# Optimization experiments

Hardware: AMD Instinct MI355X
Metric: run time of the kernel (lower is better)

Reference implementation:

```python
import jax, jax.numpy as jnp
import numpy as np

B = 2
D_MODEL = 256
D_FFN = 1024
N_LEVELS = 4
N_HEADS = 8
N_POINTS = 4
D_HEAD = D_MODEL // N_HEADS
SHAPES = np.array([[128, 128], [64, 64], [32, 32], [16, 16]], dtype=np.int32)  # (H, W) per level
LEN = int(SHAPES.prod(axis=1).sum())  # 21760
EPS = 1e-5


def _layer_norm(x, g, b):
    m = jnp.mean(x, axis=-1, keepdims=True)
    v = jnp.mean(jnp.square(x - m), axis=-1, keepdims=True)
    return (x - m) * jax.lax.rsqrt(v + EPS) * g + b


def _bilinear_gather(v_l, loc, H, W):
    # v_l: [B, H*W, NH, DH]; loc: [B, L, NH, NP, 2] in normalized [0,1] coords (x, y)
    # grid_sample(align_corners=False, padding_mode=zeros) semantics: pixel = loc * size - 0.5
    x = loc[..., 0] * W - 0.5
    y = loc[..., 1] * H - 0.5
    x0 = jnp.floor(x)
    y0 = jnp.floor(y)
    dx = x - x0
    dy = y - y0
    x0i = x0.astype(jnp.int32)
    y0i = y0.astype(jnp.int32)
    b_ix = jnp.arange(v_l.shape[0])[:, None, None, None]
    h_ix = jnp.arange(v_l.shape[2])[None, None, :, None]

    def corner(xi, yi, w):
        valid = (xi >= 0) & (xi < W) & (yi >= 0) & (yi < H)
        idx = jnp.clip(yi, 0, H - 1) * W + jnp.clip(xi, 0, W - 1)
        v = v_l[b_ix, idx, h_ix]  # [B, L, NH, NP, DH]
        return v * (w * valid.astype(v.dtype))[..., None]

    return (corner(x0i, y0i, (1 - dx) * (1 - dy))
            + corner(x0i + 1, y0i, dx * (1 - dy))
            + corner(x0i, y0i + 1, (1 - dx) * dy)
            + corner(x0i + 1, y0i + 1, dx * dy))


def _forward(src, pos, reference_points,
             w_off, b_off, w_attn, b_attn, w_val, b_val, w_out, b_out,
             ln1_g, ln1_b, w1, b1, w2, b2, ln2_g, ln2_b,
             spatial_shapes, level_start_index, padding_mask):
    shapes = np.asarray(spatial_shapes)        # static per-level (H, W)
    starts = np.asarray(level_start_index)     # static level offsets
    Bsz, L, _ = src.shape

    # ---- MSDeformAttn ----
    q = src + pos                              # with_pos_embed
    value = src @ w_val + b_val
    value = jnp.where(padding_mask[..., None], 0.0, value)
    value = value.reshape(Bsz, L, N_HEADS, D_HEAD)

    off = (q @ w_off + b_off).reshape(Bsz, L, N_HEADS, N_LEVELS, N_POINTS, 2)
    attn = (q @ w_attn + b_attn).reshape(Bsz, L, N_HEADS, N_LEVELS * N_POINTS)
    attn = jax.nn.softmax(attn, axis=-1).reshape(Bsz, L, N_HEADS, N_LEVELS, N_POINTS)

    wh = jnp.asarray(shapes[:, ::-1].copy(), dtype=src.dtype)  # [NL, 2] = (W, H)
    loc = reference_points[:, :, None, :, None, :] + off / wh[None, None, None, :, None, :]

    out = jnp.zeros((Bsz, L, N_HEADS, D_HEAD), src.dtype)
    for l in range(N_LEVELS):
        H, W = int(shapes[l, 0]), int(shapes[l, 1])
        s = int(starts[l])
        v_l = value[:, s:s + H * W]                          # [B, H*W, NH, DH]
        sampled = _bilinear_gather(v_l, loc[:, :, :, l], H, W)  # [B, L, NH, NP, DH]
        out = out + (sampled * attn[:, :, :, l][..., None]).sum(axis=3)
    attn_out = out.reshape(Bsz, L, D_MODEL) @ w_out + b_out

    # ---- residual + LN + FFN + residual + LN (dropout = identity in eval) ----
    x = _layer_norm(src + attn_out, ln1_g, ln1_b)
    ffn = jax.nn.relu(x @ w1 + b1) @ w2 + b2
    return _layer_norm(x + ffn, ln2_g, ln2_b)


def setup_inputs() -> dict:
    key = jax.random.key(0)
    ks = jax.random.split(key, 16)
    s = 0.02
    n_off = N_HEADS * N_LEVELS * N_POINTS
    level_start = np.concatenate([[0], SHAPES.prod(axis=1).cumsum()[:-1]]).astype(np.int32)
    return {
        "src": jax.random.normal(ks[0], (B, LEN, D_MODEL), jnp.float32),
        "pos": jax.random.normal(ks[1], (B, LEN, D_MODEL), jnp.float32),
        "reference_points": jax.random.uniform(ks[2], (B, LEN, N_LEVELS, 2), jnp.float32),
        "spatial_shapes": jnp.asarray(SHAPES),
        "level_start_index": jnp.asarray(level_start),
        "padding_mask": jnp.zeros((B, LEN), jnp.bool_),
        "w_off": jax.random.normal(ks[3], (D_MODEL, n_off * 2), jnp.float32) * s,
        "b_off": jax.random.normal(ks[4], (n_off * 2,), jnp.float32) * 0.5,
        "w_attn": jax.random.normal(ks[5], (D_MODEL, n_off), jnp.float32) * s,
        "b_attn": jnp.zeros((n_off,), jnp.float32),
        "w_val": jax.random.normal(ks[6], (D_MODEL, D_MODEL), jnp.float32) * s,
        "b_val": jnp.zeros((D_MODEL,), jnp.float32),
        "w_out": jax.random.normal(ks[7], (D_MODEL, D_MODEL), jnp.float32) * s,
        "b_out": jnp.zeros((D_MODEL,), jnp.float32),
        "ln1_g": jnp.ones((D_MODEL,), jnp.float32),
        "ln1_b": jnp.zeros((D_MODEL,), jnp.float32),
        "w1": jax.random.normal(ks[8], (D_MODEL, D_FFN), jnp.float32) * s,
        "b1": jnp.zeros((D_FFN,), jnp.float32),
        "w2": jax.random.normal(ks[9], (D_FFN, D_MODEL), jnp.float32) * s,
        "b2": jnp.zeros((D_MODEL,), jnp.float32),
        "ln2_g": jnp.ones((D_MODEL,), jnp.float32),
        "ln2_b": jnp.zeros((D_MODEL,), jnp.float32),
    }


def reference(src, pos, reference_points, spatial_shapes, level_start_index, padding_mask,
              w_off, b_off, w_attn, b_attn, w_val, b_val, w_out, b_out,
              ln1_g, ln1_b, w1, b1, w2, b2, ln2_g, ln2_b):
    return _forward(src, pos, reference_points,
                    w_off, b_off, w_attn, b_attn, w_val, b_val, w_out, b_out,
                    ln1_g, ln1_b, w1, b1, w2, b2, ln2_g, ln2_b,
                    spatial_shapes, level_start_index, padding_mask)
```

## Files before the change

kernel.cpp:

```cpp
#include <hip/hip_runtime.h>
#include <hip/hip_bf16.h>

#define BSZ      2
#define LTOK     21760
#define NTOK     (BSZ * LTOK)
#define DMODEL   256
#define DFFN     1024

typedef __attribute__((ext_vector_type(8))) short short8;
typedef __attribute__((ext_vector_type(4))) float f32x4;

__device__ __forceinline__ unsigned short f2bf(float x) {
    __hip_bfloat16 h = __float2bfloat16(x);
    return *reinterpret_cast<unsigned short*>(&h);
}
__device__ __forceinline__ float bf2f(unsigned short u) {
    union { unsigned int i; float f; } c; c.i = ((unsigned int)u) << 16; return c.f;
}
__device__ __forceinline__ float bflo(unsigned int u) {
    union { unsigned int i; float f; } c; c.i = u << 16; return c.f;
}
__device__ __forceinline__ float bfhi(unsigned int u) {
    union { unsigned int i; float f; } c; c.i = u & 0xffff0000u; return c.f;
}

#define TM 128
#define TN 256
#define TBK 32
#define EBS 264

__device__ __forceinline__ void gemm_core(
    const unsigned short* __restrict__ A,
    const unsigned short* __restrict__ Bt,
    unsigned short* sA, unsigned short* sB,
    int bm, int bn, int N, int K,
    int tid, int lane, int wm, int wn,
    f32x4 acc[4][8])
{
    const int sr = tid >> 6;
    const int fr = lane & 15;
    const int fk = (lane >> 4) * 8;

    for (int k0 = 0; k0 < K; k0 += TBK) {
        #pragma unroll
        for (int rr = 0; rr < 2; ++rr) {
            const int s = sr + rr * 4;
            const size_t grow = (size_t)(bm + s * 16 + fr);
            *(uint4*)&sA[s * 512 + lane * 8] = *(const uint4*)(A + grow * K + k0 + fk);
        }
        #pragma unroll
        for (int rr = 0; rr < 4; ++rr) {
            const int s = sr + rr * 4;
            int gn = bn + s * 16 + fr;
            gn = min(gn, N - 1);
            *(uint4*)&sB[s * 512 + lane * 8] = *(const uint4*)(Bt + (size_t)gn * K + k0 + fk);
        }
        __syncthreads();

        short8 af[4], bfr[8];
        #pragma unroll
        for (int i = 0; i < 4; ++i)
            af[i] = *(const short8*)&sA[(wm * 4 + i) * 512 + lane * 8];
        #pragma unroll
        for (int j = 0; j < 8; ++j)
            bfr[j] = *(const short8*)&sB[(wn * 8 + j) * 512 + lane * 8];
        #pragma unroll
        for (int i = 0; i < 4; ++i)
            #pragma unroll
            for (int j = 0; j < 8; ++j)
                acc[i][j] = __builtin_amdgcn_mfma_f32_16x16x32_bf16(
                    af[i], bfr[j], acc[i][j], 0, 0, 0);
        __syncthreads();
    }
}

__global__ __launch_bounds__(256, 2) void gemm_mfma(
    const unsigned short* __restrict__ A,
    const unsigned short* __restrict__ Bt, const float* __restrict__ bias,
    unsigned short* __restrict__ Cb,
    int M, int N, int K, int relu)
{
    __shared__ __align__(16) unsigned short smem[TM * TBK + TN * TBK];
    const int tid  = threadIdx.x;
    const int lane = tid & 63;
    const int wave = tid >> 6;
    const int wm = wave >> 1, wn = wave & 1;
    const int bm = blockIdx.y * TM;
    const int bn = blockIdx.x * TN;

    f32x4 acc[4][8];
    #pragma unroll
    for (int i = 0; i < 4; ++i)
        #pragma unroll
        for (int j = 0; j < 8; ++j)
            acc[i][j] = (f32x4){0.f, 0.f, 0.f, 0.f};

    gemm_core(A, Bt, smem, smem + TM * TBK, bm, bn, N, K, tid, lane, wm, wn, acc);

    const int r0 = (lane >> 4) * 4;
    const int c0 = lane & 15;
    unsigned short* eb = smem;
    #pragma unroll
    for (int i = 0; i < 4; ++i) {
        if (i) __syncthreads();
        #pragma unroll
        for (int j = 0; j < 8; ++j) {
            const int col = bn + wn * 128 + j * 16 + c0;
            const float bj = (col < N) ? bias[col] : 0.f;
            #pragma unroll
            for (int r = 0; r < 4; ++r) {
                float v = acc[i][j][r] + bj;
                if (relu) v = fmaxf(v, 0.f);
                eb[(wm * 16 + r0 + r) * EBS + wn * 128 + j * 16 + c0] = f2bf(v);
            }
        }
        __syncthreads();
        #pragma unroll
        for (int qq = 0; qq < 4; ++qq) {
            const int q  = tid + qq * 256;
            const int rl = q >> 5;
            const int ch = q & 31;
            const int grow = bm + (rl >> 4) * 64 + i * 16 + (rl & 15);
            const int colb = bn + ch * 8;
            if (colb < N)
                *(uint4*)&Cb[(size_t)grow * N + colb] =
                    *(const uint4*)&eb[rl * EBS + ch * 8];
        }
    }
}

__global__ __launch_bounds__(256, 2) void gemm_proj(
    const unsigned short* __restrict__ A0, const unsigned short* __restrict__ B0,
    const float* __restrict__ bias0, unsigned short* __restrict__ C0,
    const unsigned char* __restrict__ mask,
    const unsigned short* __restrict__ A1, const unsigned short* __restrict__ B1,
    const float* __restrict__ bias1, unsigned short* __restrict__ C1)
{
    __shared__ __align__(16) unsigned short smem[TM * TBK + TN * TBK];
    const int tid  = threadIdx.x;
    const int lane = tid & 63;
    const int wave = tid >> 6;
    const int wm = wave >> 1, wn = wave & 1;
    const int bm = blockIdx.y * TM;
    const int bx = blockIdx.x;

    const int isv = (bx == 0);
    const unsigned short* A    = isv ? A0 : A1;
    const unsigned short* Bt   = isv ? B0 : B1;
    const float*          bias = isv ? bias0 : bias1;
    const int N  = isv ? 256 : 384;
    const int bn = isv ? 0 : (bx - 1) * 256;
    const int K  = 256;

    f32x4 acc[4][8];
    #pragma unroll
    for (int i = 0; i < 4; ++i)
        #pragma unroll
        for (int j = 0; j < 8; ++j)
            acc[i][j] = (f32x4){0.f, 0.f, 0.f, 0.f};

    gemm_core(A, Bt, smem, smem + TM * TBK, bm, bn, N, K, tid, lane, wm, wn, acc);

    const int r0 = (lane >> 4) * 4;
    const int c0 = lane & 15;
    unsigned short* eb = smem;
    #pragma unroll
    for (int i = 0; i < 4; ++i) {
        if (i) __syncthreads();
        #pragma unroll
        for (int j = 0; j < 8; ++j) {
            const int col = bn + wn * 128 + j * 16 + c0;
            const float bj = (col < N) ? bias[col] : 0.f;
            #pragma unroll
            for (int r = 0; r < 4; ++r) {
                const int row = bm + wm * 64 + i * 16 + r0 + r;
                float v = acc[i][j][r] + bj;
                if (isv && mask[row]) v = 0.f;
                eb[(wm * 16 + r0 + r) * EBS + wn * 128 + j * 16 + c0] = f2bf(v);
            }
        }
        __syncthreads();
        #pragma unroll
        for (int qq = 0; qq < 4; ++qq) {
            const int q  = tid + qq * 256;
            const int rl = q >> 5;
            const int ch = q & 31;
            const int grow = bm + (rl >> 4) * 64 + i * 16 + (rl & 15);
            const int colb = bn + ch * 8;
            if (colb < N) {
                const uint4 val = *(const uint4*)&eb[rl * EBS + ch * 8];
                if (isv) {
                    const int bb   = grow >= LTOK;
                    const int srow = grow - bb * LTOK;
                    const int hcol = ch >> 2;
                    const int d    = (ch & 3) * 8;
                    *(uint4*)&C0[((size_t)(bb * 8 + hcol) * LTOK + srow) * 32 + d] = val;
                } else {
                    *(uint4*)&C1[(size_t)grow * 384 + colb] = val;
                }
            }
        }
    }
}

__global__ __launch_bounds__(256, 2) void gemm_ln(
    const unsigned short* __restrict__ A,
    const unsigned short* __restrict__ Bt, const float* __restrict__ bias,
    const unsigned short* __restrict__ resid,
    const float* __restrict__ g, const float* __restrict__ be,
    float* __restrict__ outF, unsigned short* __restrict__ outB, int K)
{
    __shared__ __align__(16) unsigned short smem[TM * TBK + TN * TBK];
    const int tid  = threadIdx.x;
    const int lane = tid & 63;
    const int wave = tid >> 6;
    const int wm = wave >> 1, wn = wave & 1;
    const int bm = blockIdx.y * TM;

    f32x4 acc[4][8];
    #pragma unroll
    for (int i = 0; i < 4; ++i)
        #pragma unroll
        for (int j = 0; j < 8; ++j)
            acc[i][j] = (f32x4){0.f, 0.f, 0.f, 0.f};

    gemm_core(A, Bt, smem, smem + TM * TBK, bm, 0, 256, K, tid, lane, wm, wn, acc);

    const int r0 = (lane >> 4) * 4;
    const int c0 = lane & 15;
    unsigned short* eb = smem;

    #pragma unroll
    for (int i = 0; i < 4; ++i) {
        if (i) __syncthreads();
        #pragma unroll
        for (int j = 0; j < 8; ++j) {
            const int col = wn * 128 + j * 16 + c0;
            const float bj = bias[col];
            #pragma unroll
            for (int r = 0; r < 4; ++r)
                eb[(wm * 16 + r0 + r) * EBS + col] = f2bf(acc[i][j][r] + bj);
        }
        __syncthreads();

        const int row = tid >> 3;
        const int l   = tid & 7;
        const int grow = bm + (row >> 4) * 64 + i * 16 + (row & 15);
        const unsigned short* rr = resid + (size_t)grow * 256 + l * 32;

        float s = 0.f, sq = 0.f;
        #pragma unroll
        for (int k = 0; k < 4; ++k) {
            const uint4 e = *(const uint4*)&eb[row * EBS + l * 32 + k * 8];
            const uint4 rv = *(const uint4*)(rr + k * 8);
            const unsigned int eu[4] = {e.x, e.y, e.z, e.w};
            const unsigned int ru[4] = {rv.x, rv.y, rv.z, rv.w};
            #pragma unroll
            for (int q = 0; q < 4; ++q) {
                const float v0 = bflo(eu[q]) + bflo(ru[q]);
                const float v1 = bfhi(eu[q]) + bfhi(ru[q]);
                s += v0 + v1;
                sq += v0 * v0 + v1 * v1;
            }
        }
        #pragma unroll
        for (int m = 4; m; m >>= 1) {
            s  += __shfl_xor(s, m, 8);
            sq += __shfl_xor(sq, m, 8);
        }
        const float mean = s * (1.f / 256.f);
        const float var  = sq * (1.f / 256.f) - mean * mean;
        const float rs   = rsqrtf(var + 1e-5f);

        #pragma unroll
        for (int k = 0; k < 4; ++k) {
            const int col = l * 32 + k * 8;
            const uint4 e = *(const uint4*)&eb[row * EBS + col];
            const uint4 rv = *(const uint4*)(rr + k * 8);
            const unsigned int eu[4] = {e.x, e.y, e.z, e.w};
            const unsigned int ru[4] = {rv.x, rv.y, rv.z, rv.w};
            float o[8];
            #pragma unroll
            for (int q = 0; q < 4; ++q) {
                const float g0 = g[col + q * 2],     b0 = be[col + q * 2];
                const float g1 = g[col + q * 2 + 1], b1 = be[col + q * 2 + 1];
                o[q * 2]     = (bflo(eu[q]) + bflo(ru[q]) - mean) * rs * g0 + b0;
                o[q * 2 + 1] = (bfhi(eu[q]) + bfhi(ru[q]) - mean) * rs * g1 + b1;
            }
            if (outB) {
                uint4 pk;
                pk.x = (unsigned)f2bf(o[0]) | ((unsigned)f2bf(o[1]) << 16);
                pk.y = (unsigned)f2bf(o[2]) | ((unsigned)f2bf(o[3]) << 16);
                pk.z = (unsigned)f2bf(o[4]) | ((unsigned)f2bf(o[5]) << 16);
                pk.w = (unsigned)f2bf(o[6]) | ((unsigned)f2bf(o[7]) << 16);
                *(uint4*)(outB + (size_t)grow * 256 + col) = pk;
            } else {
                float4 f0 = make_float4(o[0], o[1], o[2], o[3]);
                float4 f1 = make_float4(o[4], o[5], o[6], o[7]);
                *(float4*)(outF + (size_t)grow * 256 + col) = f0;
                *(float4*)(outF + (size_t)grow * 256 + col + 4) = f1;
            }
        }
        __syncthreads();
    }
}

__global__ __launch_bounds__(256) void prepass(
    const float* __restrict__ src, const float* __restrict__ pos,
    unsigned short* __restrict__ sb, unsigned short* __restrict__ qs)
{
    const size_t i = ((size_t)blockIdx.x * 256 + threadIdx.x) * 4;
    const float4 s = *(const float4*)(src + i);
    const float4 p = *(const float4*)(pos + i);
    ushort4 us, uq;
    us.x = f2bf(s.x); us.y = f2bf(s.y); us.z = f2bf(s.z); us.w = f2bf(s.w);
    uq.x = f2bf(s.x + p.x); uq.y = f2bf(s.y + p.y);
    uq.z = f2bf(s.z + p.z); uq.w = f2bf(s.w + p.w);
    *(ushort4*)(sb + i) = us;
    *(ushort4*)(qs + i) = uq;
}

__global__ void transpose_all(
    const float* __restrict__ w_val, const float* __restrict__ w_off,
    const float* __restrict__ w_att, const float* __restrict__ w_out,
    const float* __restrict__ w1,    const float* __restrict__ w2,
    const float* __restrict__ b_off, const float* __restrict__ b_att,
    unsigned short* __restrict__ wvalT, unsigned short* __restrict__ woaT,
    unsigned short* __restrict__ woutT, unsigned short* __restrict__ w1T,
    unsigned short* __restrict__ w2T,   float* __restrict__ bcat)
{
    const int blk = blockIdx.x;
    const int tx = threadIdx.x, ty = threadIdx.y;
    if (blk == 736) {
        const int t = ty * 32 + tx;
        bcat[t] = (t < 256) ? b_off[t] : b_att[t - 256];
        if (t + 256 < 384) bcat[t + 256] = b_att[t];
        return;
    }
    const float* W; unsigned short* Wt; int K, N, base;
    if      (blk < 64)  { W = w_val; Wt = wvalT;           K = 256;  N = 256;  base = 0;   }
    else if (blk < 128) { W = w_off; Wt = woaT;            K = 256;  N = 256;  base = 64;  }
    else if (blk < 160) { W = w_att; Wt = woaT + 256*256;  K = 256;  N = 128;  base = 128; }
    else if (blk < 224) { W = w_out; Wt = woutT;           K = 256;  N = 256;  base = 160; }
    else if (blk < 480) { W = w1;    Wt = w1T;             K = 256;  N = 1024; base = 224; }
    else                { W = w2;    Wt = w2T;             K = 1024; N = 256;  base = 480; }
    const int local = blk - base;
    const int kb = local % (K / 32);
    const int nb = local / (K / 32);
    const int k0 = kb * 32, n0 = nb * 32;

    __shared__ float t[32][33];
    #pragma unroll
    for (int i = 0; i < 32; i += 8)
        t[ty + i][tx] = W[(size_t)(k0 + ty + i) * N + n0 + tx];
    __syncthreads();
    #pragma unroll
    for (int i = 0; i < 32; i += 8)
        Wt[(size_t)(n0 + ty + i) * K + k0 + tx] = f2bf(t[tx][ty + i]);
}

__global__ __launch_bounds__(256) void sample_kernel(
    const unsigned short* __restrict__ vT, const unsigned short* __restrict__ qp,
    const float* __restrict__ ref,
    const int* __restrict__ sshapes, const int* __restrict__ lstart,
    unsigned short* __restrict__ samp)
{
    __shared__ __align__(16) int   s_o[256][4];
    __shared__ __align__(16) float s_w[256][4];

    const int blk   = blockIdx.x;
    const int plane = blk & 15;
    const int chunk = blk >> 4;
    const int b = plane >> 3;
    const int h = plane & 7;
    const int s0 = chunk * 16;
    const int t = threadIdx.x;

    {
        const int tl = t >> 4;
        const int p  = t & 15;
        const int l  = p >> 2;
        const int pp = p & 3;
        const int H = sshapes[2 * l], W = sshapes[2 * l + 1];
        const float Wf = (float)W, Hf = (float)H;
        const size_t tok = (size_t)(b * LTOK + s0 + tl);

        const float ox = bf2f(qp[tok * 384 + h * 32 + l * 8 + pp * 2 + 0]);
        const float oy = bf2f(qp[tok * 384 + h * 32 + l * 8 + pp * 2 + 1]);
        const float rx = ref[tok * 8 + l * 2 + 0];
        const float ry = ref[tok * 8 + l * 2 + 1];

        const float x = (rx + ox / Wf) * Wf - 0.5f;
        const float y = (ry + oy / Hf) * Hf - 0.5f;
        const float x0 = floorf(x), y0 = floorf(y);
        const float dx = x - x0, dy = y - y0;
        const int x0i = (int)x0, y0i = (int)y0;
        const int s = lstart[l];

        const float a = bf2f(qp[tok * 384 + 256 + h * 16 + p]);
        float mx = a;
        #pragma unroll
        for (int m = 8; m; m >>= 1) mx = fmaxf(mx, __shfl_xor(mx, m, 16));
        const float e = __expf(a - mx);
        float ssum = e;
        #pragma unroll
        for (int m = 8; m; m >>= 1) ssum += __shfl_xor(ssum, m, 16);
        const float prob = e / ssum;

        const float cw[4] = {(1.f - dx) * (1.f - dy), dx * (1.f - dy),
                             (1.f - dx) * dy,         dx * dy};
        const int cx[4] = {x0i, x0i + 1, x0i,     x0i + 1};
        const int cy[4] = {y0i, y0i,     y0i + 1, y0i + 1};
        int4   o4;
        float4 w4;
        #pragma unroll
        for (int c = 0; c < 4; ++c) {
            const bool valid = (cx[c] >= 0) & (cx[c] < W) & (cy[c] >= 0) & (cy[c] < H);
            const int xi = min(max(cx[c], 0), W - 1);
            const int yi = min(max(cy[c], 0), H - 1);
            ((int*)&o4)[c]   = (s + yi * W + xi) * 64;
            ((float*)&w4)[c] = valid ? cw[c] * prob : 0.f;
        }
        const int r = p * 16 + tl;
        *(int4*)&s_o[r][0]   = o4;
        *(float4*)&s_w[r][0] = w4;
    }
    __syncthreads();

    const int tl = t >> 4;
    const int dp = t & 15;
    const char* vp = (const char*)(vT + (size_t)plane * LTOK * 32) + dp * 4;
    float acc0 = 0.f, acc1 = 0.f;
    #pragma unroll
    for (int p = 0; p < 16; ++p) {
        const int r = p * 16 + tl;
        const int4   o4 = *(const int4*)&s_o[r][0];
        const float4 w4 = *(const float4*)&s_w[r][0];
        const unsigned int u0 = *(const unsigned int*)(vp + o4.x);
        const unsigned int u1 = *(const unsigned int*)(vp + o4.y);
        const unsigned int u2 = *(const unsigned int*)(vp + o4.z);
        const unsigned int u3 = *(const unsigned int*)(vp + o4.w);
        acc0 = fmaf(w4.x, bflo(u0), acc0); acc1 = fmaf(w4.x, bfhi(u0), acc1);
        acc0 = fmaf(w4.y, bflo(u1), acc0); acc1 = fmaf(w4.y, bfhi(u1), acc1);
        acc0 = fmaf(w4.z, bflo(u2), acc0); acc1 = fmaf(w4.z, bfhi(u2), acc1);
        acc0 = fmaf(w4.w, bflo(u3), acc0); acc1 = fmaf(w4.w, bfhi(u3), acc1);
    }
    const unsigned int o = (unsigned)f2bf(acc0) | ((unsigned)f2bf(acc1) << 16);
    *(unsigned int*)(samp + (size_t)(b * LTOK + s0 + tl) * 256 + h * 32 + dp * 2) = o;
}

extern "C" void kernel_launch(void* const* d_in, const int* in_sizes, int n_in,
                              void* d_out, int out_size, void* d_ws, size_t ws_size,
                              hipStream_t stream)
{
    const float* src   = (const float*)d_in[0];
    const float* pos   = (const float*)d_in[1];
    const float* ref   = (const float*)d_in[2];
    const int*   sshap = (const int*)d_in[3];
    const int*   lstrt = (const int*)d_in[4];
    const unsigned char* mask = (const unsigned char*)d_in[5];
    const float* w_off = (const float*)d_in[6];
    const float* b_off = (const float*)d_in[7];
    const float* w_att = (const float*)d_in[8];
    const float* b_att = (const float*)d_in[9];
    const float* w_val = (const float*)d_in[10];
    const float* b_val = (const float*)d_in[11];
    const float* w_out = (const float*)d_in[12];
    const float* b_out = (const float*)d_in[13];
    const float* ln1g  = (const float*)d_in[14];
    const float* ln1b  = (const float*)d_in[15];
    const float* w1    = (const float*)d_in[16];
    const float* b1    = (const float*)d_in[17];
    const float* w2    = (const float*)d_in[18];
    const float* b2    = (const float*)d_in[19];
    const float* ln2g  = (const float*)d_in[20];
    const float* ln2b  = (const float*)d_in[21];
    float* out = (float*)d_out;

    const size_t HSZ = (size_t)NTOK * 256 * 2;
    char* w = (char*)d_ws;
    unsigned short* qs     = (unsigned short*)w;
    unsigned short* samp16 = (unsigned short*)w;
    unsigned short* qpb    = (unsigned short*)(w + HSZ);
    unsigned short* vT     = (unsigned short*)(w + HSZ * 5 / 2);
    unsigned short* hidb   = (unsigned short*)w;
    unsigned short* sb     = (unsigned short*)(w + HSZ * 9 / 2);
    unsigned short* xb     = (unsigned short*)(w + HSZ * 11 / 2);
    char* wreg = w + HSZ * 13 / 2;
    unsigned short* wvalT  = (unsigned short*)wreg;
    unsigned short* woaT   = wvalT + 256 * 256;
    unsigned short* woutT  = woaT + 384 * 256;
    unsigned short* w1T    = woutT + 256 * 256;
    unsigned short* w2T    = w1T + 1024 * 256;
    float*          bcat   = (float*)(w2T + 256 * 1024);

    const dim3 blk(256);

    prepass<<<dim3(NTOK / 4), blk, 0, stream>>>(src, pos, sb, qs);

    transpose_all<<<dim3(737), dim3(32, 8), 0, stream>>>(
        w_val, w_off, w_att, w_out, w1, w2, b_off, b_att,
        wvalT, woaT, woutT, w1T, w2T, bcat);

    gemm_proj<<<dim3(3, NTOK / TM), blk, 0, stream>>>(
        sb, wvalT, b_val, vT, mask, qs, woaT, bcat, qpb);

    sample_kernel<<<dim3(16 * (LTOK / 16)), blk, 0, stream>>>(
        vT, qpb, ref, sshap, lstrt, samp16);

    gemm_ln<<<dim3(1, NTOK / TM), blk, 0, stream>>>(
        samp16, woutT, b_out, sb, ln1g, ln1b, nullptr, xb, 256);

    gemm_mfma<<<dim3(4, NTOK / TM), blk, 0, stream>>>(
        xb, w1T, b1, hidb, NTOK, DFFN, 256, 1);

    gemm_ln<<<dim3(1, NTOK / TM), blk, 0, stream>>>(
        hidb, w2T, b2, xb, ln2g, ln2b, out, nullptr, DFFN);
}
```

Baseline: 480.4 us.

## Replace LDS-staged GEMM tiles with direct-from-global per-wave MFMA tiles

All four GEMM kernels drop the shared-memory A/B staging loop with its block-wide barriers. Each wave now loads its 16-row A fragment and the B fragments straight from global memory (B through L2/cache) and runs MFMAs with smaller 64-row blocks. LDS is kept only as a per-wave epilogue buffer, which allows more blocks per CU and removes the __syncthreads. The cost is that B tiles are no longer shared across waves via LDS, so global/L2 traffic for weights rises, and reuse of each weight fragment goes down.

```diff
diff --git a/kernel.cpp b/kernel.cpp
--- a/kernel.cpp
+++ b/kernel.cpp
@@ -24,284 +24,243 @@
     union { unsigned int i; float f; } c; c.i = u & 0xffff0000u; return c.f;
 }
 
-#define TM 128
-#define TN 256
-#define TBK 32
-#define EBS 264
-
-__device__ __forceinline__ void gemm_core(
-    const unsigned short* __restrict__ A,
-    const unsigned short* __restrict__ Bt,
-    unsigned short* sA, unsigned short* sB,
-    int bm, int bn, int N, int K,
-    int tid, int lane, int wm, int wn,
-    f32x4 acc[4][8])
-{
-    const int sr = tid >> 6;
-    const int fr = lane & 15;
-    const int fk = (lane >> 4) * 8;
-
-    for (int k0 = 0; k0 < K; k0 += TBK) {
-        #pragma unroll
-        for (int rr = 0; rr < 2; ++rr) {
-            const int s = sr + rr * 4;
-            const size_t grow = (size_t)(bm + s * 16 + fr);
-            *(uint4*)&sA[s * 512 + lane * 8] = *(const uint4*)(A + grow * K + k0 + fk);
-        }
-        #pragma unroll
-        for (int rr = 0; rr < 4; ++rr) {
-            const int s = sr + rr * 4;
-            int gn = bn + s * 16 + fr;
-            gn = min(gn, N - 1);
-            *(uint4*)&sB[s * 512 + lane * 8] = *(const uint4*)(Bt + (size_t)gn * K + k0 + fk);
-        }
-        __syncthreads();
-
-        short8 af[4], bfr[8];
-        #pragma unroll
-        for (int i = 0; i < 4; ++i)
-            af[i] = *(const short8*)&sA[(wm * 4 + i) * 512 + lane * 8];
-        #pragma unroll
-        for (int j = 0; j < 8; ++j)
-            bfr[j] = *(const short8*)&sB[(wn * 8 + j) * 512 + lane * 8];
-        #pragma unroll
-        for (int i = 0; i < 4; ++i)
-            #pragma unroll
-            for (int j = 0; j < 8; ++j)
-                acc[i][j] = __builtin_amdgcn_mfma_f32_16x16x32_bf16(
-                    af[i], bfr[j], acc[i][j], 0, 0, 0);
-        __syncthreads();
-    }
-}
-
-__global__ __launch_bounds__(256, 2) void gemm_mfma(
-    const unsigned short* __restrict__ A,
-    const unsigned short* __restrict__ Bt, const float* __restrict__ bias,
-    unsigned short* __restrict__ Cb,
-    int M, int N, int K, int relu)
-{
-    __shared__ __align__(16) unsigned short smem[TM * TBK + TN * TBK];
-    const int tid  = threadIdx.x;
-    const int lane = tid & 63;
-    const int wave = tid >> 6;
-    const int wm = wave >> 1, wn = wave & 1;
-    const int bm = blockIdx.y * TM;
-    const int bn = blockIdx.x * TN;
-
-    f32x4 acc[4][8];
-    #pragma unroll
-    for (int i = 0; i < 4; ++i)
-        #pragma unroll
-        for (int j = 0; j < 8; ++j)
-            acc[i][j] = (f32x4){0.f, 0.f, 0.f, 0.f};
-
-    gemm_core(A, Bt, smem, smem + TM * TBK, bm, bn, N, K, tid, lane, wm, wn, acc);
-
-    const int r0 = (lane >> 4) * 4;
-    const int c0 = lane & 15;
-    unsigned short* eb = smem;
-    #pragma unroll
-    for (int i = 0; i < 4; ++i) {
-        if (i) __syncthreads();
-        #pragma unroll
-        for (int j = 0; j < 8; ++j) {
-            const int col = bn + wn * 128 + j * 16 + c0;
-            const float bj = (col < N) ? bias[col] : 0.f;
-            #pragma unroll
-            for (int r = 0; r < 4; ++r) {
-                float v = acc[i][j][r] + bj;
-                if (relu) v = fmaxf(v, 0.f);
-                eb[(wm * 16 + r0 + r) * EBS + wn * 128 + j * 16 + c0] = f2bf(v);
-            }
-        }
-        __syncthreads();
-        #pragma unroll
-        for (int qq = 0; qq < 4; ++qq) {
-            const int q  = tid + qq * 256;
-            const int rl = q >> 5;
-            const int ch = q & 31;
-            const int grow = bm + (rl >> 4) * 64 + i * 16 + (rl & 15);
-            const int colb = bn + ch * 8;
-            if (colb < N)
-                *(uint4*)&Cb[(size_t)grow * N + colb] =
-                    *(const uint4*)&eb[rl * EBS + ch * 8];
-        }
-    }
-}
-
-__global__ __launch_bounds__(256, 2) void gemm_proj(
+
+__global__ __launch_bounds__(256, 4) void gemm_proj(
     const unsigned short* __restrict__ A0, const unsigned short* __restrict__ B0,
     const float* __restrict__ bias0, unsigned short* __restrict__ C0,
     const unsigned char* __restrict__ mask,
     const unsigned short* __restrict__ A1, const unsigned short* __restrict__ B1,
     const float* __restrict__ bias1, unsigned short* __restrict__ C1)
 {
-    __shared__ __align__(16) unsigned short smem[TM * TBK + TN * TBK];
+    __shared__ __align__(16) unsigned short eb[4][16 * 136];
     const int tid  = threadIdx.x;
     const int lane = tid & 63;
     const int wave = tid >> 6;
-    const int wm = wave >> 1, wn = wave & 1;
-    const int bm = blockIdx.y * TM;
+    const int fr = lane & 15;
+    const int fk = (lane >> 4) * 8;
     const int bx = blockIdx.x;
-
-    const int isv = (bx == 0);
-    const unsigned short* A    = isv ? A0 : A1;
-    const unsigned short* Bt   = isv ? B0 : B1;
-    const float*          bias = isv ? bias0 : bias1;
-    const int N  = isv ? 256 : 384;
-    const int bn = isv ? 0 : (bx - 1) * 256;
-    const int K  = 256;
-
-    f32x4 acc[4][8];
-    #pragma unroll
-    for (int i = 0; i < 4; ++i)
+    const int arow = blockIdx.y * 64 + wave * 16;
+
+    const int isv = (bx < 2);
+    const unsigned short* A  = isv ? A0 : A1;
+    const unsigned short* Bt = isv ? B0 : B1;
+    const float* bias        = isv ? bias0 : bias1;
+    const int bn = isv ? bx * 128 : (bx - 2) * 128;
+
+    const unsigned short* aP = A + (size_t)(arow + fr) * 256 + fk;
+    const unsigned short* bP[8];
+    #pragma unroll
+    for (int j = 0; j < 8; ++j)
+        bP[j] = Bt + (size_t)(bn + j * 16 + fr) * 256 + fk;
+
+    f32x4 acc[8];
+    #pragma unroll
+    for (int j = 0; j < 8; ++j) acc[j] = (f32x4){0.f, 0.f, 0.f, 0.f};
+
+    #pragma unroll
+    for (int k0 = 0; k0 < 256; k0 += 32) {
+        const short8 a = *(const short8*)(aP + k0);
         #pragma unroll
         for (int j = 0; j < 8; ++j)
-            acc[i][j] = (f32x4){0.f, 0.f, 0.f, 0.f};
-
-    gemm_core(A, Bt, smem, smem + TM * TBK, bm, bn, N, K, tid, lane, wm, wn, acc);
-
+            acc[j] = __builtin_amdgcn_mfma_f32_16x16x32_bf16(
+                a, *(const short8*)(bP[j] + k0), acc[j], 0, 0, 0);
+    }
+
+    unsigned short* ew = &eb[wave][0];
     const int r0 = (lane >> 4) * 4;
-    const int c0 = lane & 15;
-    unsigned short* eb = smem;
-    #pragma unroll
-    for (int i = 0; i < 4; ++i) {
-        if (i) __syncthreads();
-        #pragma unroll
-        for (int j = 0; j < 8; ++j) {
-            const int col = bn + wn * 128 + j * 16 + c0;
-            const float bj = (col < N) ? bias[col] : 0.f;
-            #pragma unroll
-            for (int r = 0; r < 4; ++r) {
-                const int row = bm + wm * 64 + i * 16 + r0 + r;
-                float v = acc[i][j][r] + bj;
-                if (isv && mask[row]) v = 0.f;
-                eb[(wm * 16 + r0 + r) * EBS + wn * 128 + j * 16 + c0] = f2bf(v);
-            }
+    const int c0 = fr;
+    int mk0 = 0, mk1 = 0, mk2 = 0, mk3 = 0;
+    if (isv) {
+        mk0 = mask[arow + r0 + 0]; mk1 = mask[arow + r0 + 1];
+        mk2 = mask[arow + r0 + 2]; mk3 = mask[arow + r0 + 3];
+    }
+    #pragma unroll
+    for (int j = 0; j < 8; ++j) {
+        const float bj = bias[bn + j * 16 + c0];
+        float v0 = acc[j][0] + bj, v1 = acc[j][1] + bj;
+        float v2 = acc[j][2] + bj, v3 = acc[j][3] + bj;
+        if (mk0) v0 = 0.f;
+        if (mk1) v1 = 0.f;
+        if (mk2) v2 = 0.f;
+        if (mk3) v3 = 0.f;
+        ew[(r0 + 0) * 136 + j * 16 + c0] = f2bf(v0);
+        ew[(r0 + 1) * 136 + j * 16 + c0] = f2bf(v1);
+        ew[(r0 + 2) * 136 + j * 16 + c0] = f2bf(v2);
+        ew[(r0 + 3) * 136 + j * 16 + c0] = f2bf(v3);
+    }
+    #pragma unroll
+    for (int qq = 0; qq < 4; ++qq) {
+        const int q  = lane + qq * 64;
+        const int rl = q >> 4;
+        const int ch = q & 15;
+        const int grow = arow + rl;
+        const uint4 val = *(const uint4*)&ew[rl * 136 + ch * 8];
+        if (isv) {
+            const int cb   = bn + ch * 8;
+            const int bb   = grow >= LTOK;
+            const int srow = grow - bb * LTOK;
+            *(uint4*)&C0[((size_t)(bb * 8 + (cb >> 5)) * LTOK + srow) * 32 + (cb & 31)] = val;
+        } else {
+            *(uint4*)&C1[(size_t)grow * 384 + bn + ch * 8] = val;
         }
-        __syncthreads();
-        #pragma unroll
-        for (int qq = 0; qq < 4; ++qq) {
-            const int q  = tid + qq * 256;
-            const int rl = q >> 5;
-            const int ch = q & 31;
-            const int grow = bm + (rl >> 4) * 64 + i * 16 + (rl & 15);
-            const int colb = bn + ch * 8;
-            if (colb < N) {
-                const uint4 val = *(const uint4*)&eb[rl * EBS + ch * 8];
-                if (isv) {
-                    const int bb   = grow >= LTOK;
-                    const int srow = grow - bb * LTOK;
-                    const int hcol = ch >> 2;
-                    const int d    = (ch & 3) * 8;
-                    *(uint4*)&C0[((size_t)(bb * 8 + hcol) * LTOK + srow) * 32 + d] = val;
-                } else {
-                    *(uint4*)&C1[(size_t)grow * 384 + colb] = val;
-                }
-            }
-        }
-    }
-}
-
+    }
+}
+
+__global__ __launch_bounds__(256, 4) void ffn1_gemm(
+    const unsigned short* __restrict__ A, const unsigned short* __restrict__ Bt,
+    const float* __restrict__ bias, unsigned short* __restrict__ Cb)
+{
+    __shared__ __align__(16) unsigned short eb[4][16 * 136];
+    const int tid  = threadIdx.x;
+    const int lane = tid & 63;
+    const int wave = tid >> 6;
+    const int fr = lane & 15;
+    const int fk = (lane >> 4) * 8;
+    const int bn = blockIdx.x * 128;
+    const int arow = blockIdx.y * 64 + wave * 16;
+
+    const unsigned short* aP = A + (size_t)(arow + fr) * 256 + fk;
+    const unsigned short* bP[8];
+    #pragma unroll
+    for (int j = 0; j < 8; ++j)
+        bP[j] = Bt + (size_t)(bn + j * 16 + fr) * 256 + fk;
+
+    f32x4 acc[8];
+    #pragma unroll
+    for (int j = 0; j < 8; ++j) acc[j] = (f32x4){0.f, 0.f, 0.f, 0.f};
+
+    #pragma unroll
+    for (int k0 = 0; k0 < 256; k0 += 32) {
+        const short8 a = *(const short8*)(aP + k0);
+        #pragma unroll
+        for (int j = 0; j < 8; ++j)
+            acc[j] = __builtin_amdgcn_mfma_f32_16x16x32_bf16(
+                a, *(const short8*)(bP[j] + k0), acc[j], 0, 0, 0);
+    }
+
+    unsigned short* ew = &eb[wave][0];
+    const int r0 = (lane >> 4) * 4;
+    const int c0 = fr;
+    #pragma unroll
+    for (int j = 0; j < 8; ++j) {
+        const float bj = bias[bn + j * 16 + c0];
+        #pragma unroll
+        for (int r = 0; r < 4; ++r)
+            ew[(r0 + r) * 136 + j * 16 + c0] = f2bf(fmaxf(acc[j][r] + bj, 0.f));
+    }
+    #pragma unroll
+    for (int qq = 0; qq < 4; ++qq) {
+        const int q  = lane + qq * 64;
+        const int rl = q >> 4;
+        const int ch = q & 15;
+        *(uint4*)&Cb[(size_t)(arow + rl) * 1024 + bn + ch * 8] =
+            *(const uint4*)&ew[rl * 136 + ch * 8];
+    }
+}
+
+template<int K>
 __global__ __launch_bounds__(256, 2) void gemm_ln(
     const unsigned short* __restrict__ A,
     const unsigned short* __restrict__ Bt, const float* __restrict__ bias,
     const unsigned short* __restrict__ resid,
     const float* __restrict__ g, const float* __restrict__ be,
-    float* __restrict__ outF, unsigned short* __restrict__ outB, int K)
-{
-    __shared__ __align__(16) unsigned short smem[TM * TBK + TN * TBK];
+    float* __restrict__ outF, unsigned short* __restrict__ outB)
+{
+    __shared__ __align__(16) unsigned short eb[4][16 * 264];
     const int tid  = threadIdx.x;
     const int lane = tid & 63;
     const int wave = tid >> 6;
-    const int wm = wave >> 1, wn = wave & 1;
-    const int bm = blockIdx.y * TM;
-
-    f32x4 acc[4][8];
-    #pragma unroll
-    for (int i = 0; i < 4; ++i)
-        #pragma unroll
-        for (int j = 0; j < 8; ++j)
-            acc[i][j] = (f32x4){0.f, 0.f, 0.f, 0.f};
-
-    gemm_core(A, Bt, smem, smem + TM * TBK, bm, 0, 256, K, tid, lane, wm, wn, acc);
-
+    const int fr = lane & 15;
+    const int fk = (lane >> 4) * 8;
+    const int arow = blockIdx.x * 64 + wave * 16;
+
+    const unsigned short* aP = A + (size_t)(arow + fr) * K + fk;
+    const unsigned short* bP[16];
+    #pragma unroll
+    for (int j = 0; j < 16; ++j)
+        bP[j] = Bt + (size_t)(j * 16 + fr) * K + fk;
+
+    f32x4 acc[16];
+    #pragma unroll
+    for (int j = 0; j < 16; ++j) acc[j] = (f32x4){0.f, 0.f, 0.f, 0.f};
+
+    #pragma unroll
+    for (int k0 = 0; k0 < K; k0 += 32) {
+        const short8 a = *(const short8*)(aP + k0);
+        #pragma unroll
+        for (int j = 0; j < 16; ++j)
+            acc[j] = __builtin_amdgcn_mfma_f32_16x16x32_bf16(
+                a, *(const short8*)(bP[j] + k0), acc[j], 0, 0, 0);
+    }
+
+    unsigned short* ew = &eb[wave][0];
     const int r0 = (lane >> 4) * 4;
-    const int c0 = lane & 15;
-    unsigned short* eb = smem;
-
-    #pragma unroll
-    for (int i = 0; i < 4; ++i) {
-        if (i) __syncthreads();
-        #pragma unroll
-        for (int j = 0; j < 8; ++j) {
-            const int col = wn * 128 + j * 16 + c0;
-            const float bj = bias[col];
-            #pragma unroll
-            for (int r = 0; r < 4; ++r)
-                eb[(wm * 16 + r0 + r) * EBS + col] = f2bf(acc[i][j][r] + bj);
+    const int c0 = fr;
+    #pragma unroll
+    for (int j = 0; j < 16; ++j) {
+        const float bj = bias[j * 16 + c0];
+        #pragma unroll
+        for (int r = 0; r < 4; ++r)
+            ew[(r0 + r) * 264 + j * 16 + c0] = f2bf(acc[j][r] + bj);
+    }
+
+    const int row = lane >> 2;
+    const int l   = lane & 3;
+    const int grow = arow + row;
+    const unsigned short* rr = resid + (size_t)grow * 256 + l * 64;
+
+    float s = 0.f, sq = 0.f;
+    #pragma unroll
+    for (int k = 0; k < 8; ++k) {
+        const uint4 e  = *(const uint4*)&ew[row * 264 + l * 64 + k * 8];
+        const uint4 rv = *(const uint4*)(rr + k * 8);
+        const unsigned int eu[4] = {e.x, e.y, e.z, e.w};
+        const unsigned int ru[4] = {rv.x, rv.y, rv.z, rv.w};
+        #pragma unroll
+        for (int q = 0; q < 4; ++q) {
+            const float v0 = bflo(eu[q]) + bflo(ru[q]);
+            const float v1 = bfhi(eu[q]) + bfhi(ru[q]);
+            s += v0 + v1;
+            sq += v0 * v0 + v1 * v1;
         }
-        __syncthreads();
-
-        const int row = tid >> 3;
-        const int l   = tid & 7;
-        const int grow = bm + (row >> 4) * 64 + i * 16 + (row & 15);
-        const unsigned short* rr = resid + (size_t)grow * 256 + l * 32;
-
-        float s = 0.f, sq = 0.f;
-        #pragma unroll
-        for (int k = 0; k < 4; ++k) {
-            const uint4 e = *(const uint4*)&eb[row * EBS + l * 32 + k * 8];
-            const uint4 rv = *(const uint4*)(rr + k * 8);
-            const unsigned int eu[4] = {e.x, e.y, e.z, e.w};
-            const unsigned int ru[4] = {rv.x, rv.y, rv.z, rv.w};
-            #pragma unroll
-            for (int q = 0; q < 4; ++q) {
-                const float v0 = bflo(eu[q]) + bflo(ru[q]);
-                const float v1 = bfhi(eu[q]) + bfhi(ru[q]);
-                s += v0 + v1;
-                sq += v0 * v0 + v1 * v1;
-            }
+    }
+    #pragma unroll
+    for (int m = 2; m; m >>= 1) {
+        s  += __shfl_xor(s, m, 4);
+        sq += __shfl_xor(sq, m, 4);
+    }
+    const float mean = s * (1.f / 256.f);
+    const float var  = sq * (1.f / 256.f) - mean * mean;
+    const float rs   = rsqrtf(var + 1e-5f);
+
+    #pragma unroll
+    for (int k = 0; k < 8; ++k) {
+        const int col = l * 64 + k * 8;
+        const uint4 e  = *(const uint4*)&ew[row * 264 + col];
+        const uint4 rv = *(const uint4*)(rr + k * 8);
+        const unsigned int eu[4] = {e.x, e.y, e.z, e.w};
+        const unsigned int ru[4] = {rv.x, rv.y, rv.z, rv.w};
+        float o[8];
+        #pragma unroll
+        for (int q = 0; q < 4; ++q) {
+            const float g0 = g[col + q * 2],     b0 = be[col + q * 2];
+            const float g1 = g[col + q * 2 + 1], b1 = be[col + q * 2 + 1];
+            o[q * 2]     = (bflo(eu[q]) + bflo(ru[q]) - mean) * rs * g0 + b0;
+            o[q * 2 + 1] = (bfhi(eu[q]) + bfhi(ru[q]) - mean) * rs * g1 + b1;
         }
-        #pragma unroll
-        for (int m = 4; m; m >>= 1) {
-            s  += __shfl_xor(s, m, 8);
-            sq += __shfl_xor(sq, m, 8);
+        if (outB) {
+            uint4 pk;
+            pk.x = (unsigned)f2bf(o[0]) | ((unsigned)f2bf(o[1]) << 16);
+            pk.y = (unsigned)f2bf(o[2]) | ((unsigned)f2bf(o[3]) << 16);
+            pk.z = (unsigned)f2bf(o[4]) | ((unsigned)f2bf(o[5]) << 16);
+            pk.w = (unsigned)f2bf(o[6]) | ((unsigned)f2bf(o[7]) << 16);
+            *(uint4*)(outB + (size_t)grow * 256 + col) = pk;
+        } else {
+            float4 f0 = make_float4(o[0], o[1], o[2], o[3]);
+            float4 f1 = make_float4(o[4], o[5], o[6], o[7]);
+            *(float4*)(outF + (size_t)grow * 256 + col) = f0;
+            *(float4*)(outF + (size_t)grow * 256 + col + 4) = f1;
         }
-        const float mean = s * (1.f / 256.f);
-        const float var  = sq * (1.f / 256.f) - mean * mean;
-        const float rs   = rsqrtf(var + 1e-5f);
-
-        #pragma unroll
-        for (int k = 0; k < 4; ++k) {
-            const int col = l * 32 + k * 8;
-            const uint4 e = *(const uint4*)&eb[row * EBS + col];
-            const uint4 rv = *(const uint4*)(rr + k * 8);
-            const unsigned int eu[4] = {e.x, e.y, e.z, e.w};
-            const unsigned int ru[4] = {rv.x, rv.y, rv.z, rv.w};
-            float o[8];
-            #pragma unroll
-            for (int q = 0; q < 4; ++q) {
-                const float g0 = g[col + q * 2],     b0 = be[col + q * 2];
-                const float g1 = g[col + q * 2 + 1], b1 = be[col + q * 2 + 1];
-                o[q * 2]     = (bflo(eu[q]) + bflo(ru[q]) - mean) * rs * g0 + b0;
-                o[q * 2 + 1] = (bfhi(eu[q]) + bfhi(ru[q]) - mean) * rs * g1 + b1;
-            }
-            if (outB) {
-                uint4 pk;
-                pk.x = (unsigned)f2bf(o[0]) | ((unsigned)f2bf(o[1]) << 16);
-                pk.y = (unsigned)f2bf(o[2]) | ((unsigned)f2bf(o[3]) << 16);
-                pk.z = (unsigned)f2bf(o[4]) | ((unsigned)f2bf(o[5]) << 16);
-                pk.w = (unsigned)f2bf(o[6]) | ((unsigned)f2bf(o[7]) << 16);
-                *(uint4*)(outB + (size_t)grow * 256 + col) = pk;
-            } else {
-                float4 f0 = make_float4(o[0], o[1], o[2], o[3]);
-                float4 f1 = make_float4(o[4], o[5], o[6], o[7]);
-                *(float4*)(outF + (size_t)grow * 256 + col) = f0;
-                *(float4*)(outF + (size_t)grow * 256 + col + 4) = f1;
-            }
-        }
-        __syncthreads();
     }
 }
 
@@ -502,18 +461,18 @@
         w_val, w_off, w_att, w_out, w1, w2, b_off, b_att,
         wvalT, woaT, woutT, w1T, w2T, bcat);
 
-    gemm_proj<<<dim3(3, NTOK / TM), blk, 0, stream>>>(
+    gemm_proj<<<dim3(5, NTOK / 64), blk, 0, stream>>>(
         sb, wvalT, b_val, vT, mask, qs, woaT, bcat, qpb);
 
     sample_kernel<<<dim3(16 * (LTOK / 16)), blk, 0, stream>>>(
         vT, qpb, ref, sshap, lstrt, samp16);
 
-    gemm_ln<<<dim3(1, NTOK / TM), blk, 0, stream>>>(
-        samp16, woutT, b_out, sb, ln1g, ln1b, nullptr, xb, 256);
-
-    gemm_mfma<<<dim3(4, NTOK / TM), blk, 0, stream>>>(
-        xb, w1T, b1, hidb, NTOK, DFFN, 256, 1);
-
-    gemm_ln<<<dim3(1, NTOK / TM), blk, 0, stream>>>(
-        hidb, w2T, b2, xb, ln2g, ln2b, out, nullptr, DFFN);
-}
+    gemm_ln<256><<<dim3(NTOK / 64), blk, 0, stream>>>(
+        samp16, woutT, b_out, sb, ln1g, ln1b, nullptr, xb);
+
+    ffn1_gemm<<<dim3(8, NTOK / 64), blk, 0, stream>>>(
+        xb, w1T, b1, hidb);
+
+    gemm_ln<1024><<<dim3(NTOK / 64), blk, 0, stream>>>(
+        hidb, w2T, b2, xb, ln2g, ln2b, out, nullptr);
+}
```

Measured after the change: 811.5 us. 68.9% more time.
